# Performance work log

Hardware: AMD Instinct MI355X
Metric: run time of the kernel (lower is better)

## Reference

```python
import jax, jax.numpy as jnp
import numpy as np


def conv1x1(x, W, b):
    # x: [B,C,H,W], W: [O,C], b: [O]
    return jnp.einsum('bchw,oc->bohw', x, W) + b[None, :, None, None]


def setup_inputs() -> dict:
    key = jax.random.key(0)
    ks = jax.random.split(key, 16)
    B, C, H, W = 4, 256, 64, 64
    C4 = C // 4
    s = lambda fan_in: 1.0 / np.sqrt(fan_in)
    inp = {
        'last_frame': jax.random.normal(ks[0], (B, C, H, W), jnp.float32),
        'current_frame': jax.random.normal(ks[1], (B, C, H, W), jnp.float32),
        'future_frame': jax.random.normal(ks[2], (B, C, H, W), jnp.float32),
        'Wqk': jax.random.normal(ks[3], (C4, C), jnp.float32) * s(C),
        'bqk': jnp.zeros((C4,), jnp.float32),
        'Wkl': jax.random.normal(ks[4], (C4, C), jnp.float32) * s(C),
        'bkl': jnp.zeros((C4,), jnp.float32),
        'Wkf': jax.random.normal(ks[5], (C4, C), jnp.float32) * s(C),
        'bkf': jnp.zeros((C4,), jnp.float32),
        'Wv': jax.random.normal(ks[6], (C4, C), jnp.float32) * s(C),
        'bv': jnp.zeros((C4,), jnp.float32),
        'Wfire': jax.random.normal(ks[7], (C, C // 2), jnp.float32) * s(C // 2),
        'bfire': jnp.zeros((C,), jnp.float32),
        'bn_gamma': jnp.ones((C,), jnp.float32),
        'bn_beta': jnp.zeros((C,), jnp.float32),
        'bn_mean': jnp.zeros((C,), jnp.float32),
        'bn_var': jnp.ones((C,), jnp.float32),
    }
    return inp


def reference(last_frame, current_frame, future_frame,
              Wqk, bqk, Wkl, bkl, Wkf, bkf, Wv, bv,
              Wfire, bfire, bn_gamma, bn_beta, bn_mean, bn_var):
    B, C, H, W = current_frame.shape
    C4 = C // 4
    HW = H * W
    eps = 1e-5

    q = conv1x1(current_frame, Wqk, bqk).reshape(B, C4, HW)       # [B,C4,HW]
    kl = conv1x1(last_frame, Wkl, bkl).reshape(B, C4, HW)          # [B,C4,HW]
    kf = conv1x1(future_frame, Wkf, bkf).reshape(B, C4, HW)        # [B,C4,HW]
    v = conv1x1(current_frame, Wv, bv).reshape(B, C4, HW)          # [B,C4,HW]

    # affinity: [B, HW(query), HW(key)], softmax over key axis
    aff_l = jax.nn.softmax(jnp.einsum('bcq,bck->bqk', q, kl), axis=-1)
    aff_f = jax.nn.softmax(jnp.einsum('bcq,bck->bqk', q, kf), axis=-1)

    # out = V @ A^T : out[b,c,q] = sum_k v[b,c,k] * aff[b,q,k]
    out_l = jnp.einsum('bck,bqk->bcq', v, aff_l).reshape(B, C4, H, W)
    out_f = jnp.einsum('bck,bqk->bcq', v, aff_f).reshape(B, C4, H, W)

    fused = jnp.concatenate([out_l, out_f], axis=1)                 # [B,C/2,H,W]
    fired = conv1x1(fused, Wfire, bfire)                            # [B,C,H,W]
    # BatchNorm (inference form with running stats)
    inv = bn_gamma / jnp.sqrt(bn_var + eps)
    fired = fired * inv[None, :, None, None] + (bn_beta - bn_mean * inv)[None, :, None, None]
    return jax.nn.relu(current_frame + fired)
```

## Files before the change

kernel.cpp:

```cpp
#include <hip/hip_runtime.h>
#include <math.h>
#include <stdint.h>

#define HWN 4096
#define CIN 256
#define CQ 64
#define LOG2E 1.44269504f
#define C2OFF 56.0f

typedef __attribute__((ext_vector_type(8))) _Float16 f16x8;
typedef __attribute__((ext_vector_type(8))) short    bf16x8;
typedef __attribute__((ext_vector_type(4))) short    bf16x4;
typedef __attribute__((ext_vector_type(4))) float    f32x4;

__device__ __forceinline__ short f2bf(float f) {
  union { float f; uint32_t u; } c; c.f = f;
  uint32_t r = (c.u + 0x7FFFu + ((c.u >> 16) & 1u)) >> 16;
  return (short)(uint16_t)r;
}

__device__ __forceinline__ void stage16(const void* g, void* l) {
  __builtin_amdgcn_global_load_lds(
      (const __attribute__((address_space(1))) uint32_t*)g,
      (__attribute__((address_space(3))) uint32_t*)l, 16, 0, 0);
}

__global__ __launch_bounds__(256) void prep_kernel(
    const float* __restrict__ Wqk, const float* __restrict__ Wkl,
    const float* __restrict__ Wkf, const float* __restrict__ Wv,
    const float* __restrict__ Wfire, const float* __restrict__ bfire,
    const float* __restrict__ gamma, const float* __restrict__ beta,
    const float* __restrict__ mean,  const float* __restrict__ var,
    _Float16* __restrict__ wqk_h, _Float16* __restrict__ wkl_h,
    _Float16* __restrict__ wkf_h, _Float16* __restrict__ wv_h,
    _Float16* __restrict__ wf_h, float* __restrict__ scale, float* __restrict__ shift) {
  int gid = blockIdx.x * 256 + threadIdx.x;
  if (gid < CQ * CIN) {
    wqk_h[gid] = (_Float16)(Wqk[gid] * LOG2E);
    wkl_h[gid] = (_Float16)Wkl[gid];
    wkf_h[gid] = (_Float16)Wkf[gid];
    wv_h[gid]  = (_Float16)Wv[gid];
  }
  if (gid < CIN * 128) wf_h[gid] = (_Float16)Wfire[gid];
  if (gid < CIN) {
    float inv = gamma[gid] / sqrtf(var[gid] + 1e-5f);
    scale[gid] = inv;
    shift[gid] = (bfire[gid] - mean[gid]) * inv + beta[gid];
  }
}

__global__ __launch_bounds__(256) void proj_kernel(
    const float* __restrict__ cur, const float* __restrict__ last, const float* __restrict__ fut,
    const _Float16* __restrict__ wqk, const float* __restrict__ bqk,
    const _Float16* __restrict__ wkl, const float* __restrict__ bkl,
    const _Float16* __restrict__ wkf, const float* __restrict__ bkf,
    const _Float16* __restrict__ wv,  const float* __restrict__ bv,
    _Float16* __restrict__ q_out, _Float16* __restrict__ kl_out,
    _Float16* __restrict__ kf_out, short* __restrict__ v_out) {
  const int tid  = threadIdx.x;
  const int w    = tid >> 6;
  const int lane = tid & 63;
  const int quad = lane >> 4;
  const int l15  = lane & 15;
  const int pass = blockIdx.x >> 8;
  const int bb   = blockIdx.x & 255;
  const int b    = bb >> 6;
  const int hwt  = (bb & 63) << 6;
  const int hw   = hwt + w * 16 + l15;

  const float* X = (pass == 0) ? cur : ((pass == 1) ? last : fut);
  const float* xp = X + (size_t)b * CIN * HWN + hw;

  float xbuf[2][8];
#pragma unroll
  for (int j = 0; j < 8; ++j) xbuf[0][j] = xp[(quad * 8 + j) * HWN];

  if (pass == 0) {
    f32x4 aq[4] = {}; f32x4 av[4] = {};
#pragma unroll
    for (int k0 = 0; k0 < CIN; k0 += 32) {
      int pi = (k0 >> 5) & 1;
      if (k0 + 32 < CIN)
#pragma unroll
        for (int j = 0; j < 8; ++j)
          xbuf[pi ^ 1][j] = xp[(k0 + 32 + quad * 8 + j) * HWN];
      f16x8 bh;
#pragma unroll
      for (int j = 0; j < 8; ++j) bh[j] = (_Float16)xbuf[pi][j];
#pragma unroll
      for (int mt = 0; mt < 4; ++mt) {
        f16x8 wa = *(const f16x8*)(wqk + (mt * 16 + l15) * CIN + k0 + quad * 8);
        aq[mt] = __builtin_amdgcn_mfma_f32_16x16x32_f16(wa, bh, aq[mt], 0, 0, 0);
        f16x8 wb = *(const f16x8*)(wv + (mt * 16 + l15) * CIN + k0 + quad * 8);
        av[mt] = __builtin_amdgcn_mfma_f32_16x16x32_f16(wb, bh, av[mt], 0, 0, 0);
      }
    }
#pragma unroll
    for (int mt = 0; mt < 4; ++mt)
#pragma unroll
      for (int r = 0; r < 4; ++r) {
        int oc = mt * 16 + quad * 4 + r;
        q_out[(b * CQ + oc) * HWN + hw] = (_Float16)(aq[mt][r] + bqk[oc] * LOG2E);
        v_out[(b * CQ + oc) * HWN + hw] = f2bf(av[mt][r] + bv[oc]);
      }
  } else {
    const _Float16* W = (pass == 1) ? wkl : wkf;
    const float* BI = (pass == 1) ? bkl : bkf;
    _Float16* OUT = (pass == 1) ? kl_out : kf_out;
    f32x4 a[4] = {};
#pragma unroll
    for (int k0 = 0; k0 < CIN; k0 += 32) {
      int pi = (k0 >> 5) & 1;
      if (k0 + 32 < CIN)
#pragma unroll
        for (int j = 0; j < 8; ++j)
          xbuf[pi ^ 1][j] = xp[(k0 + 32 + quad * 8 + j) * HWN];
      f16x8 bh;
#pragma unroll
      for (int j = 0; j < 8; ++j) bh[j] = (_Float16)xbuf[pi][j];
#pragma unroll
      for (int mt = 0; mt < 4; ++mt) {
        f16x8 wa = *(const f16x8*)(W + (mt * 16 + l15) * CIN + k0 + quad * 8);
        a[mt] = __builtin_amdgcn_mfma_f32_16x16x32_f16(wa, bh, a[mt], 0, 0, 0);
      }
    }
#pragma unroll
    for (int mt = 0; mt < 4; ++mt)
#pragma unroll
      for (int r = 0; r < 4; ++r) {
        int oc = mt * 16 + quad * 4 + r;
        OUT[(b * HWN + hw) * CQ + oc] = (_Float16)(a[mt][r] + BI[oc]);
      }
  }
}

__global__ __launch_bounds__(256, 1) void attn_kernel(
    const _Float16* __restrict__ qbuf, const _Float16* __restrict__ klbuf,
    const _Float16* __restrict__ kfbuf, const short* __restrict__ vbuf,
    _Float16* __restrict__ fused) {
  const int tid  = threadIdx.x;
  const int w    = tid >> 6;
  const int lane = tid & 63;
  const int quad = lane >> 4;
  const int l15  = lane & 15;
  const int bx   = blockIdx.x;
  const int pair = bx & 1;
  const int b    = (bx >> 1) & 3;
  const int qt   = (bx >> 3) << 7;

  const _Float16* K  = (pair ? kfbuf : klbuf) + (size_t)b * HWN * CQ;
  const short*    Vg = vbuf + (size_t)b * CQ * HWN;

  __shared__ __align__(16) _Float16 Kt[2][64][64];
  __shared__ __align__(16) short    Vt[2][64][64];
  __shared__ __align__(16) short    Pl[4][2][16][72];

  const int qbase = qt + w * 32;
  f16x8 qfrag[2][2];
#pragma unroll
  for (int i = 0; i < 2; ++i)
#pragma unroll
    for (int kk = 0; kk < 2; ++kk)
#pragma unroll
      for (int j = 0; j < 8; ++j)
        qfrag[i][kk][j] = qbuf[(b * CQ + kk * 32 + quad * 8 + j) * HWN + qbase + i * 16 + l15];

  f32x4 Oacc[2][4] = {};
  float psum[2] = {0.f, 0.f};

  auto stageK = [&](int buf, int t) {
    const _Float16* g0 = K + (size_t)(t * 64 + w * 16) * CQ + (lane >> 3) * CQ + (lane & 7) * 8;
#pragma unroll
    for (int r = 0; r < 2; ++r)
      stage16(g0 + r * 8 * CQ, &Kt[buf][w * 16 + r * 8][0]);
  };
  auto stageV = [&](int buf, int t) {
    const short* g0 = Vg + (size_t)(w * 16 + (lane >> 3)) * HWN + t * 64 + (lane & 7) * 8;
#pragma unroll
    for (int r = 0; r < 2; ++r)
      stage16(g0 + r * 8 * HWN, &Vt[buf][w * 16 + r * 8][0]);
  };

  auto body = [&](int buf) {
    f16x8 kf[4][2];
#pragma unroll
    for (int nt = 0; nt < 4; ++nt)
#pragma unroll
      for (int kk = 0; kk < 2; ++kk)
        kf[nt][kk] = *(const f16x8*)&Kt[buf][nt * 16 + l15][kk * 32 + quad * 8];
    bf16x8 vf[4][2];
#pragma unroll
    for (int ct = 0; ct < 4; ++ct)
#pragma unroll
      for (int kk = 0; kk < 2; ++kk)
        vf[ct][kk] = *(const bf16x8*)&Vt[buf][ct * 16 + l15][kk * 32 + quad * 8];
    f32x4 ST[2][4] = {};
#pragma unroll
    for (int i = 0; i < 2; ++i)
#pragma unroll
      for (int nt = 0; nt < 4; ++nt)
#pragma unroll
        for (int kk = 0; kk < 2; ++kk)
          ST[i][nt] = __builtin_amdgcn_mfma_f32_16x16x32_f16(kf[nt][kk], qfrag[i][kk], ST[i][nt], 0, 0, 0);
#pragma unroll
    for (int i = 0; i < 2; ++i)
#pragma unroll
      for (int nt = 0; nt < 4; ++nt) {
        bf16x4 pw;
#pragma unroll
        for (int r = 0; r < 4; ++r) {
          float p = __builtin_amdgcn_exp2f(ST[i][nt][r] - C2OFF);
          uint32_t u = __float_as_uint(p) & 0xffff0000u;
          psum[i] += __uint_as_float(u);
          pw[r] = (short)(u >> 16);
        }
        *(bf16x4*)&Pl[w][i][l15][nt * 16 + quad * 4] = pw;
      }
#pragma unroll
    for (int i = 0; i < 2; ++i)
#pragma unroll
      for (int kk = 0; kk < 2; ++kk) {
        bf16x8 pf = *(const bf16x8*)&Pl[w][i][l15][kk * 32 + quad * 8];
#pragma unroll
        for (int ct = 0; ct < 4; ++ct)
          Oacc[i][ct] = __builtin_amdgcn_mfma_f32_16x16x32_bf16(pf, vf[ct][kk], Oacc[i][ct], 0, 0, 0);
      }
  };

  stageK(0, 0); stageV(0, 0);
  __syncthreads();
#pragma unroll 1
  for (int tt = 0; tt < 64; tt += 2) {
    stageK(1, tt + 1); stageV(1, tt + 1);
    body(0);
    __syncthreads();
    if (tt + 2 < 64) { stageK(0, tt + 2); stageV(0, tt + 2); }
    body(1);
    __syncthreads();
  }

#pragma unroll
  for (int i = 0; i < 2; ++i) {
    psum[i] += __shfl_xor(psum[i], 16);
    psum[i] += __shfl_xor(psum[i], 32);
  }

#pragma unroll
  for (int i = 0; i < 2; ++i)
#pragma unroll
    for (int r = 0; r < 4; ++r) {
      float lt = __shfl(psum[i], quad * 4 + r);
      float invl = __builtin_amdgcn_rcpf(lt);
      int qi = qbase + i * 16 + quad * 4 + r;
#pragma unroll
      for (int ct = 0; ct < 4; ++ct)
        fused[((size_t)b * HWN + qi) * 128 + pair * 64 + ct * 16 + l15] =
            (_Float16)(Oacc[i][ct][r] * invl);
    }
}

__global__ __launch_bounds__(256) void fire_kernel(
    const _Float16* __restrict__ fused, const _Float16* __restrict__ wf,
    const float* __restrict__ scale, const float* __restrict__ shift,
    const float* __restrict__ cur, float* __restrict__ out) {
  const int tid  = threadIdx.x;
  const int w    = tid >> 6;
  const int lane = tid & 63;
  const int quad = lane >> 4;
  const int l15  = lane & 15;
  const int g    = blockIdx.x & 3;
  const int bb   = blockIdx.x >> 2;
  const int b    = bb >> 6;
  const int hwt  = (bb & 63) << 6;
  const int hwb  = hwt + w * 16;

  float curv[4][4];
#pragma unroll
  for (int mt = 0; mt < 4; ++mt)
#pragma unroll
    for (int r = 0; r < 4; ++r)
      curv[mt][r] = cur[(b * CIN + g * 64 + mt * 16 + quad * 4 + r) * HWN + hwb + l15];

  f16x8 bfr[4];
#pragma unroll
  for (int k0 = 0; k0 < 4; ++k0)
    bfr[k0] = *(const f16x8*)(fused + ((size_t)b * HWN + hwb + l15) * 128 + k0 * 32 + quad * 8);

  f32x4 acc[4] = {};
#pragma unroll
  for (int k0 = 0; k0 < 4; ++k0)
#pragma unroll
    for (int mt = 0; mt < 4; ++mt) {
      f16x8 af = *(const f16x8*)(wf + (g * 64 + mt * 16 + l15) * 128 + k0 * 32 + quad * 8);
      acc[mt] = __builtin_amdgcn_mfma_f32_16x16x32_f16(af, bfr[k0], acc[mt], 0, 0, 0);
    }

#pragma unroll
  for (int mt = 0; mt < 4; ++mt)
#pragma unroll
    for (int r = 0; r < 4; ++r) {
      int oc = g * 64 + mt * 16 + quad * 4 + r;
      int idx = (b * CIN + oc) * HWN + hwb + l15;
      float y = curv[mt][r] + acc[mt][r] * scale[oc] + shift[oc];
      out[idx] = fmaxf(y, 0.f);
    }
}

extern "C" void kernel_launch(void* const* d_in, const int* in_sizes, int n_in,
                              void* d_out, int out_size, void* d_ws, size_t ws_size,
                              hipStream_t stream) {
  const float* last  = (const float*)d_in[0];
  const float* cur   = (const float*)d_in[1];
  const float* fut   = (const float*)d_in[2];
  const float* Wqk   = (const float*)d_in[3];
  const float* bqk   = (const float*)d_in[4];
  const float* Wkl   = (const float*)d_in[5];
  const float* bkl   = (const float*)d_in[6];
  const float* Wkf   = (const float*)d_in[7];
  const float* bkf   = (const float*)d_in[8];
  const float* Wv    = (const float*)d_in[9];
  const float* bv    = (const float*)d_in[10];
  const float* Wfire = (const float*)d_in[11];
  const float* bfire = (const float*)d_in[12];
  const float* gamma = (const float*)d_in[13];
  const float* beta  = (const float*)d_in[14];
  const float* mean  = (const float*)d_in[15];
  const float* var   = (const float*)d_in[16];

  char* ws = (char*)d_ws;
  _Float16* qb     = (_Float16*)(ws);
  _Float16* klb    = (_Float16*)(ws + (2u << 20));
  _Float16* kfb    = (_Float16*)(ws + (4u << 20));
  short*    vb     = (short*)   (ws + (6u << 20));
  _Float16* fusedb = (_Float16*)(ws + (8u << 20));
  char* wsm = ws + (12u << 20);
  _Float16* wqk_h = (_Float16*)(wsm);
  _Float16* wkl_h = (_Float16*)(wsm + (32u << 10));
  _Float16* wkf_h = (_Float16*)(wsm + (64u << 10));
  _Float16* wv_h  = (_Float16*)(wsm + (96u << 10));
  _Float16* wf_h  = (_Float16*)(wsm + (128u << 10));
  float*    scale = (float*)   (wsm + (192u << 10));
  float*    shift = (float*)   (wsm + (193u << 10));
  float*    out   = (float*)d_out;

  prep_kernel<<<128, 256, 0, stream>>>(Wqk, Wkl, Wkf, Wv, Wfire, bfire,
                                       gamma, beta, mean, var,
                                       wqk_h, wkl_h, wkf_h, wv_h, wf_h, scale, shift);
  proj_kernel<<<768, 256, 0, stream>>>(cur, last, fut, wqk_h, bqk, wkl_h, bkl,
                                       wkf_h, bkf, wv_h, bv, qb, klb, kfb, vb);
  attn_kernel<<<256, 256, 0, stream>>>(qb, klb, kfb, vb, fusedb);
  fire_kernel<<<1024, 256, 0, stream>>>(fusedb, wf_h, scale, shift, cur, out);
}
```

Before: 232.4 us.

## Halve attention query tile per block, double grid, and XOR-swizzle K/V LDS

The attention kernel now gives each wave 16 query rows instead of 32 and launches 512 blocks instead of 256. This fills more of the MI355X's compute units and allows two blocks per CU. It also applies an XOR swizzle to the K and V tiles staged into LDS, so fragment reads avoid bank conflicts. The cost is that each K/V tile loaded from global memory is reused across half as many queries, which doubles K/V traffic.

```diff
diff --git a/kernel.cpp b/kernel.cpp
--- a/kernel.cpp
+++ b/kernel.cpp
@@ -134,7 +134,7 @@
   }
 }
 
-__global__ __launch_bounds__(256, 1) void attn_kernel(
+__global__ __launch_bounds__(256, 2) void attn_kernel(
     const _Float16* __restrict__ qbuf, const _Float16* __restrict__ klbuf,
     const _Float16* __restrict__ kfbuf, const short* __restrict__ vbuf,
     _Float16* __restrict__ fused) {
@@ -146,39 +146,40 @@
   const int bx   = blockIdx.x;
   const int pair = bx & 1;
   const int b    = (bx >> 1) & 3;
-  const int qt   = (bx >> 3) << 7;
+  const int qt   = (bx >> 3) << 6;
 
   const _Float16* K  = (pair ? kfbuf : klbuf) + (size_t)b * HWN * CQ;
   const short*    Vg = vbuf + (size_t)b * CQ * HWN;
 
   __shared__ __align__(16) _Float16 Kt[2][64][64];
   __shared__ __align__(16) short    Vt[2][64][64];
-  __shared__ __align__(16) short    Pl[4][2][16][72];
-
-  const int qbase = qt + w * 32;
-  f16x8 qfrag[2][2];
-#pragma unroll
-  for (int i = 0; i < 2; ++i)
-#pragma unroll
-    for (int kk = 0; kk < 2; ++kk)
-#pragma unroll
-      for (int j = 0; j < 8; ++j)
-        qfrag[i][kk][j] = qbuf[(b * CQ + kk * 32 + quad * 8 + j) * HWN + qbase + i * 16 + l15];
-
-  f32x4 Oacc[2][4] = {};
-  float psum[2] = {0.f, 0.f};
+  __shared__ __align__(16) short    Pl[4][16][72];
+
+  const int qbase = qt + w * 16;
+  f16x8 qfrag[2];
+#pragma unroll
+  for (int kk = 0; kk < 2; ++kk)
+#pragma unroll
+    for (int j = 0; j < 8; ++j)
+      qfrag[kk][j] = qbuf[(b * CQ + kk * 32 + quad * 8 + j) * HWN + qbase + l15];
+
+  f32x4 Oacc[4] = {};
+  float psum = 0.f;
+
+  const int swz = (lane & 7) ^ ((lane >> 3) & 7);
+  const int rswz = l15 & 7;
 
   auto stageK = [&](int buf, int t) {
-    const _Float16* g0 = K + (size_t)(t * 64 + w * 16) * CQ + (lane >> 3) * CQ + (lane & 7) * 8;
 #pragma unroll
     for (int r = 0; r < 2; ++r)
-      stage16(g0 + r * 8 * CQ, &Kt[buf][w * 16 + r * 8][0]);
+      stage16(K + (size_t)(t * 64 + w * 16 + r * 8 + (lane >> 3)) * CQ + swz * 8,
+              &Kt[buf][w * 16 + r * 8][0]);
   };
   auto stageV = [&](int buf, int t) {
-    const short* g0 = Vg + (size_t)(w * 16 + (lane >> 3)) * HWN + t * 64 + (lane & 7) * 8;
 #pragma unroll
     for (int r = 0; r < 2; ++r)
-      stage16(g0 + r * 8 * HWN, &Vt[buf][w * 16 + r * 8][0]);
+      stage16(Vg + (size_t)(w * 16 + r * 8 + (lane >> 3)) * HWN + t * 64 + swz * 8,
+              &Vt[buf][w * 16 + r * 8][0]);
   };
 
   auto body = [&](int buf) {
@@ -187,44 +188,38 @@
     for (int nt = 0; nt < 4; ++nt)
 #pragma unroll
       for (int kk = 0; kk < 2; ++kk)
-        kf[nt][kk] = *(const f16x8*)&Kt[buf][nt * 16 + l15][kk * 32 + quad * 8];
+        kf[nt][kk] = *(const f16x8*)&Kt[buf][nt * 16 + l15][((kk * 4 + quad) ^ rswz) * 8];
     bf16x8 vf[4][2];
 #pragma unroll
     for (int ct = 0; ct < 4; ++ct)
 #pragma unroll
       for (int kk = 0; kk < 2; ++kk)
-        vf[ct][kk] = *(const bf16x8*)&Vt[buf][ct * 16 + l15][kk * 32 + quad * 8];
-    f32x4 ST[2][4] = {};
-#pragma unroll
-    for (int i = 0; i < 2; ++i)
-#pragma unroll
-      for (int nt = 0; nt < 4; ++nt)
-#pragma unroll
-        for (int kk = 0; kk < 2; ++kk)
-          ST[i][nt] = __builtin_amdgcn_mfma_f32_16x16x32_f16(kf[nt][kk], qfrag[i][kk], ST[i][nt], 0, 0, 0);
-#pragma unroll
-    for (int i = 0; i < 2; ++i)
-#pragma unroll
-      for (int nt = 0; nt < 4; ++nt) {
-        bf16x4 pw;
-#pragma unroll
-        for (int r = 0; r < 4; ++r) {
-          float p = __builtin_amdgcn_exp2f(ST[i][nt][r] - C2OFF);
-          uint32_t u = __float_as_uint(p) & 0xffff0000u;
-          psum[i] += __uint_as_float(u);
-          pw[r] = (short)(u >> 16);
-        }
-        *(bf16x4*)&Pl[w][i][l15][nt * 16 + quad * 4] = pw;
-      }
-#pragma unroll
-    for (int i = 0; i < 2; ++i)
-#pragma unroll
-      for (int kk = 0; kk < 2; ++kk) {
-        bf16x8 pf = *(const bf16x8*)&Pl[w][i][l15][kk * 32 + quad * 8];
-#pragma unroll
-        for (int ct = 0; ct < 4; ++ct)
-          Oacc[i][ct] = __builtin_amdgcn_mfma_f32_16x16x32_bf16(pf, vf[ct][kk], Oacc[i][ct], 0, 0, 0);
-      }
+        vf[ct][kk] = *(const bf16x8*)&Vt[buf][ct * 16 + l15][((kk * 4 + quad) ^ rswz) * 8];
+    f32x4 ST[4] = {};
+#pragma unroll
+    for (int nt = 0; nt < 4; ++nt)
+#pragma unroll
+      for (int kk = 0; kk < 2; ++kk)
+        ST[nt] = __builtin_amdgcn_mfma_f32_16x16x32_f16(kf[nt][kk], qfrag[kk], ST[nt], 0, 0, 0);
+#pragma unroll
+    for (int nt = 0; nt < 4; ++nt) {
+      bf16x4 pw;
+#pragma unroll
+      for (int r = 0; r < 4; ++r) {
+        float p = __builtin_amdgcn_exp2f(ST[nt][r] - C2OFF);
+        uint32_t u = __float_as_uint(p) & 0xffff0000u;
+        psum += __uint_as_float(u);
+        pw[r] = (short)(u >> 16);
+      }
+      *(bf16x4*)&Pl[w][l15][nt * 16 + quad * 4] = pw;
+    }
+#pragma unroll
+    for (int kk = 0; kk < 2; ++kk) {
+      bf16x8 pf = *(const bf16x8*)&Pl[w][l15][kk * 32 + quad * 8];
+#pragma unroll
+      for (int ct = 0; ct < 4; ++ct)
+        Oacc[ct] = __builtin_amdgcn_mfma_f32_16x16x32_bf16(pf, vf[ct][kk], Oacc[ct], 0, 0, 0);
+    }
   };
 
   stageK(0, 0); stageV(0, 0);
@@ -239,24 +234,19 @@
     __syncthreads();
   }
 
-#pragma unroll
-  for (int i = 0; i < 2; ++i) {
-    psum[i] += __shfl_xor(psum[i], 16);
-    psum[i] += __shfl_xor(psum[i], 32);
-  }
-
-#pragma unroll
-  for (int i = 0; i < 2; ++i)
-#pragma unroll
-    for (int r = 0; r < 4; ++r) {
-      float lt = __shfl(psum[i], quad * 4 + r);
-      float invl = __builtin_amdgcn_rcpf(lt);
-      int qi = qbase + i * 16 + quad * 4 + r;
-#pragma unroll
-      for (int ct = 0; ct < 4; ++ct)
-        fused[((size_t)b * HWN + qi) * 128 + pair * 64 + ct * 16 + l15] =
-            (_Float16)(Oacc[i][ct][r] * invl);
-    }
+  psum += __shfl_xor(psum, 16);
+  psum += __shfl_xor(psum, 32);
+
+#pragma unroll
+  for (int r = 0; r < 4; ++r) {
+    float lt = __shfl(psum, quad * 4 + r);
+    float invl = __builtin_amdgcn_rcpf(lt);
+    int qi = qbase + quad * 4 + r;
+#pragma unroll
+    for (int ct = 0; ct < 4; ++ct)
+      fused[((size_t)b * HWN + qi) * 128 + pair * 64 + ct * 16 + l15] =
+          (_Float16)(Oacc[ct][r] * invl);
+  }
 }
 
 __global__ __launch_bounds__(256) void fire_kernel(
@@ -348,6 +338,6 @@
                                        wqk_h, wkl_h, wkf_h, wv_h, wf_h, scale, shift);
   proj_kernel<<<768, 256, 0, stream>>>(cur, last, fut, wqk_h, bqk, wkl_h, bkl,
                                        wkf_h, bkf, wv_h, bv, qb, klb, kfb, vb);
-  attn_kernel<<<256, 256, 0, stream>>>(qb, klb, kfb, vb, fusedb);
+  attn_kernel<<<512, 256, 0, stream>>>(qb, klb, kfb, vb, fusedb);
   fire_kernel<<<1024, 256, 0, stream>>>(fusedb, wf_h, scale, shift, cur, out);
 }
```

New measurement: 206.6 us. 11.1% less time.
